# Optimization experiments

Hardware: AMD Instinct MI355X
Metric: run time of the kernel (lower is better)

## Reference

```python
import jax, jax.numpy as jnp
import numpy as np

T = 2048        # q_len (current chunk)
P = 2048        # past KV cache length
HID = 4096      # hidden_size
H = 32          # num_attention_heads
D = HID // H    # head_dim = 128
THETA = 10000.0


def apply_rope(x, pos):
    # x: [H, T, D], pos: [T] int
    half = D // 2
    inv_freq = 1.0 / (THETA ** (jnp.arange(0, half, dtype=jnp.float32) / half))
    ang = pos.astype(jnp.float32)[:, None] * inv_freq[None, :]      # [T, D/2]
    cos = jnp.concatenate([jnp.cos(ang), jnp.cos(ang)], axis=-1)[None]  # [1, T, D]
    sin = jnp.concatenate([jnp.sin(ang), jnp.sin(ang)], axis=-1)[None]
    rot = jnp.concatenate([-x[..., half:], x[..., :half]], axis=-1)
    return x * cos + rot * sin


def setup_inputs() -> dict:
    key = jax.random.key(0)
    ks = jax.random.split(key, 8)
    s = 1.0 / np.sqrt(HID)
    inp = {
        "hidden_states": jax.random.normal(ks[0], (T, HID), dtype=jnp.float32),
        "attention_mask": jnp.triu(jnp.full((T, T), -jnp.inf, dtype=jnp.float32), k=1),
        "Wq": jax.random.normal(ks[1], (HID, HID), dtype=jnp.float32) * s,
        "Wk": jax.random.normal(ks[2], (HID, HID), dtype=jnp.float32) * s,
        "Wv": jax.random.normal(ks[3], (HID, HID), dtype=jnp.float32) * s,
        "Wo": jax.random.normal(ks[4], (HID, HID), dtype=jnp.float32) * s,
        "past_k": jax.random.normal(ks[5], (H, P, D), dtype=jnp.float32),
        "past_v": jax.random.normal(ks[6], (H, P, D), dtype=jnp.float32),
        "position_ids": P + jnp.arange(T, dtype=jnp.int32),
        "past_length": P,
    }
    return inp


def reference(hidden_states, attention_mask, Wq, Wk, Wv, Wo, past_k, past_v,
              position_ids, past_length):
    # QKV projections -> [H, T, D]
    proj = lambda W: (hidden_states @ W).reshape(T, H, D).transpose(1, 0, 2)
    q, k, v = proj(Wq), proj(Wk), proj(Wv)
    q = apply_rope(q, position_ids)
    k = apply_rope(k, position_ids)

    scale = 1.0 / jnp.sqrt(jnp.float32(D))
    # scores against past cache and current chunk (fp32 softmax, as in source)
    past_dots = (jnp.einsum('htd,hsd->hts', q, past_k) * scale).astype(jnp.float32)
    pmask = jnp.where(jnp.arange(P) < past_length, 0.0, -jnp.inf)  # [P]
    past_dots = past_dots + pmask
    cur = ((jnp.einsum('htd,hsd->hts', q, k) * scale) + attention_mask).astype(jnp.float32)

    # online-softmax merge via logsumexp combination
    past_lse = jax.scipy.special.logsumexp(past_dots, axis=-1, keepdims=True)
    cur_lse = jax.scipy.special.logsumexp(cur, axis=-1, keepdims=True)
    tot_lse = jnp.logaddexp(past_lse, cur_lse)
    pw = jnp.exp(past_dots - tot_lse).astype(q.dtype)
    cw = jnp.exp(cur - tot_lse).astype(q.dtype)

    out = jnp.einsum('hts,hsd->htd', pw, past_v) + jnp.einsum('hts,hsd->htd', cw, v)
    out = jnp.where(past_length == 0,
                    jnp.einsum('hts,hsd->htd', jax.nn.softmax(cur, axis=-1).astype(q.dtype), v),
                    out)
    out = out.transpose(1, 0, 2).reshape(T, HID)   # [T, hidden]
    return out @ Wo
```

## Files before the change

### kernel.cpp

```cpp
#include <hip/hip_runtime.h>
#include <cstdint>
#include <cstddef>

#define T_LEN 2048
#define PAST_MAX 2048
#define HID 4096
#define NHEAD 32
#define DHEAD 128

typedef __bf16 bf16_t;
typedef __bf16 bf16x4 __attribute__((ext_vector_type(4)));
typedef __bf16 bf16x8 __attribute__((ext_vector_type(8)));
typedef float  f32x4  __attribute__((ext_vector_type(4)));
typedef float  f32x16 __attribute__((ext_vector_type(16)));
typedef unsigned int u32x4 __attribute__((ext_vector_type(4)));

__device__ __forceinline__ void gload16(const void* g, void* l){
  __builtin_amdgcn_global_load_lds((const __attribute__((address_space(1))) void*)g,
                                   (__attribute__((address_space(3))) void*)l,
                                   16, 0, 0);
}

__device__ __forceinline__ unsigned pack_bf16(float a, float b){
  const unsigned ua = __builtin_bit_cast(unsigned short, (bf16_t)a);
  const unsigned ub = __builtin_bit_cast(unsigned short, (bf16_t)b);
  return ua | (ub << 16);
}

__global__ void cvt2_k(const float* __restrict__ a, bf16_t* __restrict__ ao,
                       const float* __restrict__ b, bf16_t* __restrict__ bo, int n4){
  int i = blockIdx.x * 256 + threadIdx.x;
  if (i < n4){
    const float4 v = ((const float4*)a)[i];
    bf16x4 o = { (bf16_t)v.x, (bf16_t)v.y, (bf16_t)v.z, (bf16_t)v.w };
    ((bf16x4*)ao)[i] = o;
  } else {
    i -= n4;
    const float4 v = ((const float4*)b)[i];
    bf16x4 o = { (bf16_t)v.x, (bf16_t)v.y, (bf16_t)v.z, (bf16_t)v.w };
    ((bf16x4*)bo)[i] = o;
  }
}

__global__ __launch_bounds__(256) void transpose2_k(const float* __restrict__ in,
                                                    bf16_t* __restrict__ out, int R, int C){
  __shared__ float tile[64][65];
  const int r0 = blockIdx.x << 6, c0 = blockIdx.y << 6;
  const size_t bo = (size_t)blockIdx.z * (size_t)R * (size_t)C;
  const int tx = threadIdx.x & 15, ty = threadIdx.x >> 4;
#pragma unroll
  for (int k = 0; k < 4; ++k){
    const float4 v = *(const float4*)(in + bo + (size_t)(r0 + ty + 16*k) * C + c0 + tx*4);
    float* tp = &tile[ty + 16*k][tx*4];
    tp[0] = v.x; tp[1] = v.y; tp[2] = v.z; tp[3] = v.w;
  }
  __syncthreads();
  const int rr0 = (threadIdx.x & 7) * 8;
  const int ccb = threadIdx.x >> 3;
#pragma unroll
  for (int k = 0; k < 2; ++k){
    const int cc = ccb + 32*k;
    bf16x8 o;
#pragma unroll
    for (int j = 0; j < 8; ++j) o[j] = (bf16_t)tile[rr0 + j][cc];
    *(bf16x8*)(out + bo + (size_t)(c0 + cc) * R + r0 + rr0) = o;
  }
}

__global__ __launch_bounds__(256) void transpose3_k(
    const float* __restrict__ s0, const float* __restrict__ s1, const float* __restrict__ s2,
    bf16_t* __restrict__ d0, bf16_t* __restrict__ d1, bf16_t* __restrict__ d2){
  __shared__ float tile[64][65];
  const float* in = (blockIdx.z == 0) ? s0 : (blockIdx.z == 1) ? s1 : s2;
  bf16_t* out = (blockIdx.z == 0) ? d0 : (blockIdx.z == 1) ? d1 : d2;
  const int r0 = blockIdx.x << 6, c0 = blockIdx.y << 6;
  const int tx = threadIdx.x & 15, ty = threadIdx.x >> 4;
#pragma unroll
  for (int k = 0; k < 4; ++k){
    const float4 v = *(const float4*)(in + (size_t)(r0 + ty + 16*k) * HID + c0 + tx*4);
    float* tp = &tile[ty + 16*k][tx*4];
    tp[0] = v.x; tp[1] = v.y; tp[2] = v.z; tp[3] = v.w;
  }
  __syncthreads();
  const int rr0 = (threadIdx.x & 7) * 8;
  const int ccb = threadIdx.x >> 3;
#pragma unroll
  for (int k = 0; k < 2; ++k){
    const int cc = ccb + 32*k;
    bf16x8 o;
#pragma unroll
    for (int j = 0; j < 8; ++j) o[j] = (bf16_t)tile[rr0 + j][cc];
    *(bf16x8*)(out + (size_t)(c0 + cc) * HID + r0 + rr0) = o;
  }
}

__global__ void ropek_k(bf16_t* __restrict__ K, const int* __restrict__ pos){
  const int idx = blockIdx.x * 256 + threadIdx.x;
  const int i = idx & 63;
  const int t = (idx >> 6) & (T_LEN - 1);
  const int h = idx >> 17;
  const size_t base = ((size_t)h * T_LEN + t) * DHEAD;
  const float p = (float)pos[t];
  const float inv = __expf(-(float)i * 0.14391156605212898f);
  const float ang = p * inv;
  float sn, cs;
  sincosf(ang, &sn, &cs);
  const float b0 = (float)K[base + i], b1 = (float)K[base + i + 64];
  K[base + i]      = (bf16_t)(b0 * cs - b1 * sn);
  K[base + i + 64] = (bf16_t)(b1 * cs + b0 * sn);
}

#define QUAD16(AH, NH, BF) \
  __builtin_amdgcn_s_setprio(1); \
  _Pragma("unroll") \
  for (int kk = 0; kk < 2; ++kk){ \
    _Pragma("unroll") \
    for (int mf = 0; mf < 4; ++mf){ \
      _Pragma("unroll") \
      for (int ni = 0; ni < 2; ++ni) \
        acc[(AH)*4 + mf][(NH)*2 + ni] = __builtin_amdgcn_mfma_f32_16x16x32_bf16( \
            af[mf][kk], BF[ni][kk], acc[(AH)*4 + mf][(NH)*2 + ni], 0, 0, 0); \
    } \
  } \
  __builtin_amdgcn_s_setprio(0);

__global__ __launch_bounds__(512, 1) void gemmqkv8_k(
    const bf16_t* __restrict__ A,
    const bf16_t* __restrict__ B0p, const bf16_t* __restrict__ B1p, const bf16_t* __restrict__ B2p,
    bf16_t* __restrict__ OQ, bf16_t* __restrict__ OK2, bf16_t* __restrict__ OVT, int cpx)
{
  const int bid = blockIdx.x;
  const int wg  = (bid & 7) * cpx + (bid >> 3);
  const int mt  = wg & 7;
  const int nt  = wg >> 3;
  const int z   = nt >> 4;
  const int m0  = mt << 8;
  const int n0  = (nt & 15) << 8;
  const bf16_t* __restrict__ B = (z == 0) ? B0p : (z == 1) ? B1p : B2p;

  const int tid = threadIdx.x;
  const int wv = tid >> 6, lane = tid & 63, lm = lane & 15, g = lane >> 4;
  const int wr = wv >> 2, wc = wv & 3;

  __shared__ __align__(16) char smem[131072];

  const f32x4 fzero = {0.f, 0.f, 0.f, 0.f};
  f32x4 acc[8][4];
#pragma unroll
  for (int i = 0; i < 8; ++i)
#pragma unroll
    for (int j = 0; j < 4; ++j) acc[i][j] = fzero;

  int arow_[2], brow_[2], jcol_[2];
#pragma unroll
  for (int i = 0; i < 2; ++i){
    const int c  = i * 512 + tid;
    const int rl = c >> 3;
    const int j  = (c & 7) ^ (rl & 7);
    arow_[i] = m0 + ((rl >> 6) << 7) + (rl & 63);
    brow_[i] = n0 + ((rl >> 5) << 6) + (rl & 31);
    jcol_[i] = j << 3;
  }
  const int ldst0 = ((0 * 512 + wv * 64) << 4);
  const int ldst1 = ((1 * 512 + wv * 64) << 4);

  auto stgA = [&](int kt, int ah){
    if ((unsigned)kt < 64u){
      char* dst = smem + (kt & 1) * 65536 + ah * 16384;
      const bf16_t* base = A + (size_t)kt * 64;
      gload16(base + (size_t)(arow_[0] + ah * 64) * HID + jcol_[0], dst + ldst0);
      gload16(base + (size_t)(arow_[1] + ah * 64) * HID + jcol_[1], dst + ldst1);
    }
  };
  auto stgB = [&](int kt, int nh){
    if ((unsigned)kt < 64u){
      char* dst = smem + (kt & 1) * 65536 + 32768 + nh * 16384;
      const bf16_t* base = B + (size_t)kt * 64;
      gload16(base + (size_t)(brow_[0] + nh * 32) * HID + jcol_[0], dst + ldst0);
      gload16(base + (size_t)(brow_[1] + nh * 32) * HID + jcol_[1], dst + ldst1);
    }
  };

  const int koff0 = ((0 + g) ^ (lm & 7)) << 4;
  const int koff1 = ((4 + g) ^ (lm & 7)) << 4;
  const int abase = ((wr << 6) + lm) << 7;
  const int bbase = ((wc << 5) + lm) << 7;

  stgA(0, 0); stgB(0, 0); stgB(0, 1); stgA(0, 1);
  stgA(1, 0); stgB(1, 0); stgB(1, 1);
  asm volatile("s_waitcnt vmcnt(6)" ::: "memory");
  __builtin_amdgcn_s_barrier();

  bf16x8 af[4][2], b0f[2][2], b1f[2][2];

  for (int kt = 0; kt < 64; ++kt){
    char* buf = smem + (kt & 1) * 65536;

#pragma unroll
    for (int mf = 0; mf < 4; ++mf){
      af[mf][0] = *(const bf16x8*)(buf + abase + mf * 2048 + koff0);
      af[mf][1] = *(const bf16x8*)(buf + abase + mf * 2048 + koff1);
    }
#pragma unroll
    for (int ni = 0; ni < 2; ++ni){
      b0f[ni][0] = *(const bf16x8*)(buf + 32768 + bbase + ni * 2048 + koff0);
      b0f[ni][1] = *(const bf16x8*)(buf + 32768 + bbase + ni * 2048 + koff1);
    }
    stgA(kt + 1, 1);
    __builtin_amdgcn_sched_barrier(0);
    __builtin_amdgcn_s_barrier();
    asm volatile("s_waitcnt lgkmcnt(0)" ::: "memory");
    __builtin_amdgcn_sched_barrier(0);
    QUAD16(0, 0, b0f)
    __builtin_amdgcn_s_barrier();

#pragma unroll
    for (int ni = 0; ni < 2; ++ni){
      b1f[ni][0] = *(const bf16x8*)(buf + 49152 + bbase + ni * 2048 + koff0);
      b1f[ni][1] = *(const bf16x8*)(buf + 49152 + bbase + ni * 2048 + koff1);
    }
    stgA(kt + 2, 0);
    __builtin_amdgcn_sched_barrier(0);
    __builtin_amdgcn_s_barrier();
    asm volatile("s_waitcnt lgkmcnt(0)" ::: "memory");
    __builtin_amdgcn_sched_barrier(0);
    QUAD16(0, 1, b1f)
    __builtin_amdgcn_s_barrier();

#pragma unroll
    for (int mf = 0; mf < 4; ++mf){
      af[mf][0] = *(const bf16x8*)(buf + 16384 + abase + mf * 2048 + koff0);
      af[mf][1] = *(const bf16x8*)(buf + 16384 + abase + mf * 2048 + koff1);
    }
    stgB(kt + 2, 0);
    __builtin_amdgcn_sched_barrier(0);
    __builtin_amdgcn_s_barrier();
    asm volatile("s_waitcnt lgkmcnt(0)" ::: "memory");
    __builtin_amdgcn_sched_barrier(0);
    QUAD16(1, 1, b1f)
    __builtin_amdgcn_s_barrier();

    stgB(kt + 2, 1);
    if (kt < 60) asm volatile("s_waitcnt vmcnt(6)" ::: "memory");
    else         asm volatile("s_waitcnt vmcnt(0)" ::: "memory");
    __builtin_amdgcn_sched_barrier(0);
    __builtin_amdgcn_s_barrier();
    QUAD16(1, 0, b0f)
    __builtin_amdgcn_s_barrier();
  }

#pragma unroll
  for (int ni4 = 0; ni4 < 4; ++ni4){
    const int col = n0 + wc * 64 + (ni4 >> 1) * 32 + (ni4 & 1) * 16 + lm;
    const int hh = col >> 7, dd = col & 127;
#pragma unroll
    for (int mf8 = 0; mf8 < 8; ++mf8){
      const int trow0 = m0 + wr * 128 + (mf8 >> 2) * 64 + (mf8 & 3) * 16 + g * 4;
      if (z == 2){
        bf16x4 v4 = { (bf16_t)acc[mf8][ni4][0], (bf16_t)acc[mf8][ni4][1],
                      (bf16_t)acc[mf8][ni4][2], (bf16_t)acc[mf8][ni4][3] };
        *(bf16x4*)(OVT + ((size_t)hh * DHEAD + dd) * T_LEN + trow0) = v4;
      } else {
        bf16_t* ob = (z == 1) ? OK2 : OQ;
#pragma unroll
        for (int r = 0; r < 4; ++r)
          ob[((size_t)hh * T_LEN + trow0 + r) * DHEAD + dd] = (bf16_t)acc[mf8][ni4][r];
      }
    }
  }
}

__global__ __launch_bounds__(512, 1) void gemm4p_k(
    const bf16_t* __restrict__ A, const bf16_t* __restrict__ B,
    float* __restrict__ OF, int cpx)
{
  const int bid = blockIdx.x;
  const int wg  = (bid & 7) * cpx + (bid >> 3);
  const int mt  = wg & 7;
  const int nt  = wg >> 3;
  const int m0  = mt << 8;
  const int n0  = nt << 7;

  const int tid = threadIdx.x;
  const int wv = tid >> 6, lane = tid & 63, lm = lane & 15, g = lane >> 4;
  const int wr = wv >> 1, wc = wv & 1;

  __shared__ __align__(16) char smem[98304];

  const f32x4 fzero = {0.f, 0.f, 0.f, 0.f};
  f32x4 acc[4][4];
#pragma unroll
  for (int i = 0; i < 4; ++i)
#pragma unroll
    for (int j = 0; j < 4; ++j) acc[i][j] = fzero;

  int srow[2], schk[2];
#pragma unroll
  for (int i = 0; i < 2; ++i){
    const int c = i * 512 + tid;
    srow[i] = c >> 3;
    schk[i] = (c & 7) ^ (srow[i] & 7);
  }
  const int sdst0 = ((0 * 512 + wv * 64) << 4);
  const int sdst1 = ((1 * 512 + wv * 64) << 4);

  auto stg = [&](int kt, int op){
    if (kt < 64){
      char* dst = smem + (kt & 1) * 49152 + op * 16384;
      const bf16_t* base = (op < 2) ? A + (size_t)(m0 + (op << 7)) * HID
                                    : B + (size_t)n0 * HID;
      base += kt * 64;
      gload16(base + (size_t)srow[0] * HID + schk[0] * 8, dst + sdst0);
      gload16(base + (size_t)srow[1] * HID + schk[1] * 8, dst + sdst1);
    }
  };

  const int koff0 = ((g)     ^ (lm & 7)) << 4;
  const int koff1 = ((4 + g) ^ (lm & 7)) << 4;
  const int abase = ((wr >> 1) << 14) + ((((wr & 1) << 6) + lm) << 7);
  const int bbase = 32768 + ((((wc << 6)) + lm) << 7);

  bf16x8 bfr[4][2];
  auto dsB = [&](int buf){
    const char* p = smem + buf * 49152 + bbase;
#pragma unroll
    for (int ni = 0; ni < 4; ++ni){
      bfr[ni][0] = *(const bf16x8*)(p + ni * 2048 + koff0);
      bfr[ni][1] = *(const bf16x8*)(p + ni * 2048 + koff1);
    }
  };

  stg(0, 2);
  stg(0, 0); stg(0, 1);
  stg(1, 2);
  asm volatile("s_waitcnt vmcnt(2)" ::: "memory");
  __builtin_amdgcn_s_barrier();

  for (int t = 0; t < 32; ++t){
    const int c0 = 2 * t, c1 = 2 * t + 1;
    const bool last = (t == 31);

#pragma unroll
    for (int half = 0; half < 2; ++half){
      const char* bufp = smem + half * 49152;
      bf16x8 afr[2][2];
      dsB(half);
#pragma unroll
      for (int mf = 0; mf < 2; ++mf){
        afr[mf][0] = *(const bf16x8*)(bufp + abase + mf * 2048 + koff0);
        afr[mf][1] = *(const bf16x8*)(bufp + abase + mf * 2048 + koff1);
      }
      if (half == 0){ stg(c1, 0); stg(c1, 1); }
      else          { stg(c0 + 2, 0); stg(c0 + 2, 1); }
      __builtin_amdgcn_s_barrier();
      asm volatile("s_waitcnt lgkmcnt(0)" ::: "memory");
      __builtin_amdgcn_s_setprio(1);
#pragma unroll
      for (int kk = 0; kk < 2; ++kk)
#pragma unroll
        for (int mf = 0; mf < 2; ++mf)
#pragma unroll
          for (int ni = 0; ni < 4; ++ni)
            acc[mf][ni] = __builtin_amdgcn_mfma_f32_16x16x32_bf16(afr[mf][kk], bfr[ni][kk], acc[mf][ni], 0, 0, 0);
      __builtin_amdgcn_s_setprio(0);
      __builtin_amdgcn_s_barrier();

#pragma unroll
      for (int mf = 0; mf < 2; ++mf){
        afr[mf][0] = *(const bf16x8*)(bufp + abase + (mf + 2) * 2048 + koff0);
        afr[mf][1] = *(const bf16x8*)(bufp + abase + (mf + 2) * 2048 + koff1);
      }
      if (half == 0) stg(c0 + 2, 2);
      else           stg(c1 + 2, 2);
      if (last) asm volatile("s_waitcnt vmcnt(0)" ::: "memory");
      else      asm volatile("s_waitcnt vmcnt(2)" ::: "memory");
      __builtin_amdgcn_s_barrier();
      asm volatile("s_waitcnt lgkmcnt(0)" ::: "memory");
      __builtin_amdgcn_s_setprio(1);
#pragma unroll
      for (int kk = 0; kk < 2; ++kk)
#pragma unroll
        for (int mf = 0; mf < 2; ++mf)
#pragma unroll
          for (int ni = 0; ni < 4; ++ni)
            acc[mf + 2][ni] = __builtin_amdgcn_mfma_f32_16x16x32_bf16(afr[mf][kk], bfr[ni][kk], acc[mf + 2][ni], 0, 0, 0);
      __builtin_amdgcn_s_setprio(0);
      __builtin_amdgcn_s_barrier();
    }
  }

#pragma unroll
  for (int ni = 0; ni < 4; ++ni){
    const int col = n0 + wc * 64 + ni * 16 + lm;
#pragma unroll
    for (int mf = 0; mf < 4; ++mf)
#pragma unroll
      for (int r = 0; r < 4; ++r){
        const int trow = m0 + wr * 64 + mf * 16 + g * 4 + r;
        OF[(size_t)trow * HID + col] = acc[mf][ni][r];
      }
  }
}

__global__ __launch_bounds__(256, 2) void attn2_k(
    const bf16_t* __restrict__ Q,
    const bf16_t* __restrict__ Kc,
    const bf16_t* __restrict__ VTc,
    const bf16_t* __restrict__ Kp,
    const bf16_t* __restrict__ VTp,
    bf16_t* __restrict__ Ctx,
    const int* __restrict__ plen_p,
    const int* __restrict__ pos)
{
  const int bid = blockIdx.x;
  const int xcd = bid & 7;
  const int k   = bid >> 3;
  const int ho  = k >> 4;
  const int qraw= k & 15;
  const int h   = (xcd << 2) | ho;
  const int qb  = (ho & 2) ? (15 - qraw) : qraw;

  const int tid = threadIdx.x;
  const int w = tid >> 6, lane = tid & 63, l31 = lane & 31, hi = lane >> 5;
  const int qw0 = qb * 128 + w * 32;
  const int qrow = qw0 + l31;
  const int plen = plen_p[0];
  const int npast = (plen + 63) >> 6;
  const int NT = npast + 2 * qb + 2;

  __shared__ __align__(16) char smem[65536 + 512];
  float* lred = (float*)(smem + 65536);

  const bf16_t* qbase = Q + ((size_t)h * T_LEN + qrow) * DHEAD;
  bf16x8 qf[8];
#pragma unroll
  for (int dc = 0; dc < 8; ++dc)
    qf[dc] = *(const bf16x8*)(qbase + dc * 16 + 8 * hi);
  {
    const float ppos = (float)pos[qrow];
    const float qs = 0.08838834764831845f;
#pragma unroll
    for (int dc = 0; dc < 4; ++dc)
#pragma unroll
      for (int j = 0; j < 8; ++j){
        const int fi = dc * 16 + 8 * hi + j;
        const float invf = __expf(-(float)fi * 0.14391156605212898f);
        float sn, cs;
        sincosf(ppos * invf, &sn, &cs);
        const float a0 = (float)qf[dc][j], a1 = (float)qf[dc + 4][j];
        qf[dc][j]     = (bf16_t)((a0 * cs - a1 * sn) * qs);
        qf[dc + 4][j] = (bf16_t)((a1 * cs + a0 * sn) * qs);
      }
  }
  __builtin_amdgcn_sched_barrier(0);

  const f32x16 fz = {0.f,0.f,0.f,0.f,0.f,0.f,0.f,0.f,0.f,0.f,0.f,0.f,0.f,0.f,0.f,0.f};
  f32x16 o[4] = {fz, fz, fz, fz};
  float m = -1e30f, l = 0.f;

  auto stage = [&](int t, int buf){
    const bf16_t* kb; const bf16_t* vb;
    if (t < npast){
      const int s0 = t * 64;
      kb = Kp  + ((size_t)h * PAST_MAX + s0) * DHEAD;
      vb = VTp + (size_t)h * DHEAD * PAST_MAX + s0;
    } else {
      const int s0 = (t - npast) * 64;
      kb = Kc  + ((size_t)h * T_LEN + s0) * DHEAD;
      vb = VTc + (size_t)h * DHEAD * T_LEN + s0;
    }
    char* kl = smem + buf * 32768;
    char* vl = kl + 16384;
#pragma unroll
    for (int i = 0; i < 4; ++i){
      const int c = i * 256 + w * 64 + lane;
      const int krow = c >> 4, kcol = c & 15;
      gload16(kb + (size_t)krow * DHEAD + ((kcol ^ (krow & 7)) << 3), kl + (i * 256 + w * 64) * 16);
      const int vrow = c >> 3, vcol = c & 7;
      gload16(vb + (size_t)vrow * 2048 + ((vcol ^ (vrow & 7)) << 3), vl + (i * 256 + w * 64) * 16);
    }
  };

  stage(0, 0);
  __builtin_amdgcn_sched_barrier(0);

  for (int t = 0; t < NT; ++t){
    const int cur = t & 1;
    if (t + 1 < NT){
      stage(t + 1, cur ^ 1);
      asm volatile("s_waitcnt vmcnt(8)" ::: "memory");
    } else {
      asm volatile("s_waitcnt vmcnt(0)" ::: "memory");
    }
    __builtin_amdgcn_sched_barrier(0);
    __builtin_amdgcn_s_barrier();
    __builtin_amdgcn_sched_barrier(0);

    const bool isc = (t >= npast);
    const int s0c = (t - npast) * 64;
    const bool active = !isc || (s0c <= qw0 + 31);

    if (active){
      char* kl = smem + cur * 32768;
      char* vl = kl + 16384;

      f32x16 sacc[2] = {fz, fz};
      __builtin_amdgcn_s_setprio(1);
#pragma unroll
      for (int kvh = 0; kvh < 2; ++kvh){
        const int krow = (kvh << 5) + l31;
        const int kbo = krow << 8;
        const int sw = (krow & 7) << 4;
#pragma unroll
        for (int dc = 0; dc < 8; ++dc){
          const bf16x8 kf = *(const bf16x8*)(kl + kbo + ((dc * 32 + 16 * hi) ^ sw));
          sacc[kvh] = __builtin_amdgcn_mfma_f32_32x32x16_bf16(kf, qf[dc], sacc[kvh], 0, 0, 0);
        }
      }
      __builtin_amdgcn_s_setprio(0);

      const bool mcur  = isc && (s0c + 63 > qw0);
      const bool mpast = !isc && ((t + 1) * 64 > plen);
      float pv[2][16];
      float pm = -1e30f;
      if (mcur | mpast){
#pragma unroll
        for (int kvh = 0; kvh < 2; ++kvh)
#pragma unroll
          for (int r = 0; r < 16; ++r){
            float x = sacc[kvh][r];
            const int kvoff = (kvh << 5) + (r & 3) + 8 * (r >> 2) + 4 * hi;
            if (mcur  && (s0c + kvoff >  qrow)) x = -1e30f;
            if (mpast && (t * 64 + kvoff >= plen)) x = -1e30f;
            pv[kvh][r] = x;
            pm = fmaxf(pm, x);
          }
      } else {
#pragma unroll
        for (int kvh = 0; kvh < 2; ++kvh)
#pragma unroll
          for (int r = 0; r < 16; ++r){
            pv[kvh][r] = sacc[kvh][r];
            pm = fmaxf(pm, sacc[kvh][r]);
          }
      }
      pm = fmaxf(pm, __shfl_xor(pm, 32));

      if (!__all(pm - m <= 8.f)){
        const float mn = fmaxf(m, pm);
        const float corr = __expf(m - mn);
        m = mn;
        l *= corr;
        if (hi == 0) lred[(w << 5) + l31] = corr;
        asm volatile("s_waitcnt lgkmcnt(0)" ::: "memory");
#pragma unroll
        for (int r = 0; r < 16; ++r){
          const float cc = lred[(w << 5) + (r & 3) + 8 * (r >> 2) + 4 * hi];
#pragma unroll
          for (int nb = 0; nb < 4; ++nb) o[nb][r] *= cc;
        }
      }

      float sum = 0.f;
#pragma unroll
      for (int kvh = 0; kvh < 2; ++kvh)
#pragma unroll
        for (int r = 0; r < 16; ++r){
          const float pe = __expf(pv[kvh][r] - m);
          pv[kvh][r] = pe;
          sum += pe;
        }
      sum += __shfl_xor(sum, 32);
      l += sum;

      unsigned wds[2][8];
#pragma unroll
      for (int kvh = 0; kvh < 2; ++kvh)
#pragma unroll
        for (int i = 0; i < 8; ++i)
          wds[kvh][i] = pack_bf16(pv[kvh][2 * i], pv[kvh][2 * i + 1]);

      bf16x8 pf[4];
#pragma unroll
      for (int ks = 0; ks < 4; ++ks){
        const int s = ks & 1, kvh = ks >> 1;
        const unsigned a0 = hi ? wds[kvh][4 * s]     : wds[kvh][4 * s + 2];
        const unsigned a1 = hi ? wds[kvh][4 * s + 1] : wds[kvh][4 * s + 3];
        const unsigned z0 = (unsigned)__shfl_xor((int)a0, 32);
        const unsigned z1 = (unsigned)__shfl_xor((int)a1, 32);
        u32x4 fw;
        fw[0] = hi ? z0 : wds[kvh][4 * s];
        fw[1] = hi ? z1 : wds[kvh][4 * s + 1];
        fw[2] = hi ? wds[kvh][4 * s + 2] : z0;
        fw[3] = hi ? wds[kvh][4 * s + 3] : z1;
        pf[ks] = __builtin_bit_cast(bf16x8, fw);
      }

      __builtin_amdgcn_s_setprio(1);
#pragma unroll
      for (int ks = 0; ks < 4; ++ks)
#pragma unroll
        for (int nb = 0; nb < 4; ++nb){
          const int vrow = (nb << 5) + l31;
          const bf16x8 vf = *(const bf16x8*)(vl + (vrow << 7) + ((ks * 32 + 16 * hi) ^ ((vrow & 7) << 4)));
          o[nb] = __builtin_amdgcn_mfma_f32_32x32x16_bf16(pf[ks], vf, o[nb], 0, 0, 0);
        }
      __builtin_amdgcn_s_setprio(0);
    }
    __builtin_amdgcn_sched_barrier(0);
    __builtin_amdgcn_s_barrier();
  }

  if (hi == 0) lred[(w << 5) + l31] = l;
  asm volatile("s_waitcnt lgkmcnt(0)" ::: "memory");
#pragma unroll
  for (int r = 0; r < 16; ++r){
    const int cr = (r & 3) + 8 * (r >> 2) + 4 * hi;
    const float li = 1.f / lred[(w << 5) + cr];
    const int trow = qw0 + cr;
    bf16_t* cb = Ctx + (size_t)trow * HID + h * DHEAD + l31;
#pragma unroll
    for (int nb = 0; nb < 4; ++nb)
      cb[nb << 5] = (bf16_t)(o[nb][r] * li);
  }
}

extern "C" void kernel_launch(void* const* d_in, const int* in_sizes, int n_in,
                              void* d_out, int out_size, void* d_ws, size_t ws_size,
                              hipStream_t stream)
{
  const float* X   = (const float*)d_in[0];
  const float* Wq  = (const float*)d_in[2];
  const float* Wk  = (const float*)d_in[3];
  const float* Wv  = (const float*)d_in[4];
  const float* Wo  = (const float*)d_in[5];
  const float* PKi = (const float*)d_in[6];
  const float* PVi = (const float*)d_in[7];
  const int* POS   = (const int*)d_in[8];
  const int* PLEN  = (const int*)d_in[9];
  float* OUT = (float*)d_out;

  char* ws = (char*)d_ws;
  const size_t SZ_XB  = (size_t)T_LEN * HID * 2;
  const size_t SZ_W   = (size_t)HID * HID * 2;
  const size_t SZ_HTD = (size_t)NHEAD * T_LEN * DHEAD * 2;

  bf16_t* XB  = (bf16_t*)(ws);
  bf16_t* WT0 = (bf16_t*)(ws + SZ_XB);
  bf16_t* WT1 = (bf16_t*)(ws + SZ_XB + SZ_W);
  bf16_t* WT2 = (bf16_t*)(ws + SZ_XB + 2 * SZ_W);
  char* p = ws + SZ_XB + 3 * SZ_W;
  bf16_t* QB   = (bf16_t*)p; p += SZ_HTD;
  bf16_t* KB   = (bf16_t*)p; p += SZ_HTD;
  bf16_t* VTB  = (bf16_t*)p; p += SZ_HTD;
  bf16_t* KPB  = (bf16_t*)p; p += SZ_HTD;
  bf16_t* VPTB = (bf16_t*)p; p += SZ_HTD;
  bf16_t* CTX  = (bf16_t*)p; p += SZ_HTD;
  bf16_t* WOT  = QB;

  dim3 blk256(256);
  dim3 blk512(512);
  cvt2_k<<<16384, blk256, 0, stream>>>(X, XB, PKi, KPB, T_LEN * HID / 4);
  transpose3_k<<<dim3(64,64,3), blk256, 0, stream>>>(Wq, Wk, Wv, WT0, WT1, WT2);
  transpose2_k<<<dim3(32,2,32), blk256, 0, stream>>>(PVi, VPTB, PAST_MAX, DHEAD);

  gemmqkv8_k<<<384, blk512, 0, stream>>>(XB, WT0, WT1, WT2, QB, KB, VTB, 48);
  ropek_k<<<16384, blk256, 0, stream>>>(KB, POS);
  attn2_k<<<512, blk256, 0, stream>>>(QB, KB, VTB, KPB, VPTB, CTX, PLEN, POS);

  transpose2_k<<<dim3(64,64,1), blk256, 0, stream>>>(Wo, WOT, HID, HID);
  gemm4p_k<<<256, blk512, 0, stream>>>(CTX, WOT, OUT, 32);
}
```

Measured before the change: 562.8 us.

## Retile fused QKV GEMM to 128x384 tiles over concatenated weights

The QKV projection GEMM moves from 256x256 tiles (384 blocks) to 128x384 tiles (512 blocks), treating the three transposed weight matrices as one contiguous N=12288 operand. Each k-step loads one A slice and three B slices, and the output column decides whether results go to Q, K, or transposed V. The goal is better load balance across the CUs, since 512 blocks divide more evenly than 384, at the cost of lower arithmetic intensity per tile. It relies on WT0, WT1 and WT2 sitting contiguously in the workspace.

Result: faster. 535.4 us (-4.9%).

```diff
diff --git a/kernel.cpp b/kernel.cpp
--- a/kernel.cpp
+++ b/kernel.cpp
@@ -110,7 +110,7 @@
   K[base + i + 64] = (bf16_t)(b1 * cs + b0 * sn);
 }
 
-#define QUAD16(AH, NH, BF) \
+#define QUAD384(PR, BF) \
   __builtin_amdgcn_s_setprio(1); \
   _Pragma("unroll") \
   for (int kk = 0; kk < 2; ++kk){ \
@@ -118,25 +118,23 @@
     for (int mf = 0; mf < 4; ++mf){ \
       _Pragma("unroll") \
       for (int ni = 0; ni < 2; ++ni) \
-        acc[(AH)*4 + mf][(NH)*2 + ni] = __builtin_amdgcn_mfma_f32_16x16x32_bf16( \
-            af[mf][kk], BF[ni][kk], acc[(AH)*4 + mf][(NH)*2 + ni], 0, 0, 0); \
+        acc[mf][(PR)*2 + ni] = __builtin_amdgcn_mfma_f32_16x16x32_bf16( \
+            af[mf][kk], BF[ni][kk], acc[mf][(PR)*2 + ni], 0, 0, 0); \
     } \
   } \
   __builtin_amdgcn_s_setprio(0);
 
-__global__ __launch_bounds__(512, 1) void gemmqkv8_k(
+__global__ __launch_bounds__(512, 1) void gemmqkv384_k(
     const bf16_t* __restrict__ A,
-    const bf16_t* __restrict__ B0p, const bf16_t* __restrict__ B1p, const bf16_t* __restrict__ B2p,
-    bf16_t* __restrict__ OQ, bf16_t* __restrict__ OK2, bf16_t* __restrict__ OVT, int cpx)
+    const bf16_t* __restrict__ Bc,
+    bf16_t* __restrict__ OQ, bf16_t* __restrict__ OK2, bf16_t* __restrict__ OVT)
 {
   const int bid = blockIdx.x;
-  const int wg  = (bid & 7) * cpx + (bid >> 3);
-  const int mt  = wg & 7;
-  const int nt  = wg >> 3;
-  const int z   = nt >> 4;
-  const int m0  = mt << 8;
-  const int n0  = (nt & 15) << 8;
-  const bf16_t* __restrict__ B = (z == 0) ? B0p : (z == 1) ? B1p : B2p;
+  const int wg  = (bid & 7) * 64 + (bid >> 3);
+  const int mt  = wg & 15;
+  const int nt  = wg >> 4;
+  const int m0  = mt << 7;
+  const int n0g = nt * 384;
 
   const int tid = threadIdx.x;
   const int wv = tid >> 6, lane = tid & 63, lm = lane & 15, g = lane >> 4;
@@ -145,40 +143,35 @@
   __shared__ __align__(16) char smem[131072];
 
   const f32x4 fzero = {0.f, 0.f, 0.f, 0.f};
-  f32x4 acc[8][4];
-#pragma unroll
-  for (int i = 0; i < 8; ++i)
-#pragma unroll
-    for (int j = 0; j < 4; ++j) acc[i][j] = fzero;
-
-  int arow_[2], brow_[2], jcol_[2];
+  f32x4 acc[4][6];
+#pragma unroll
+  for (int i = 0; i < 4; ++i)
+#pragma unroll
+    for (int j = 0; j < 6; ++j) acc[i][j] = fzero;
+
+  size_t aoff[2], boff[2];
 #pragma unroll
   for (int i = 0; i < 2; ++i){
-    const int c  = i * 512 + tid;
-    const int rl = c >> 3;
-    const int j  = (c & 7) ^ (rl & 7);
-    arow_[i] = m0 + ((rl >> 6) << 7) + (rl & 63);
-    brow_[i] = n0 + ((rl >> 5) << 6) + (rl & 31);
-    jcol_[i] = j << 3;
-  }
-  const int ldst0 = ((0 * 512 + wv * 64) << 4);
-  const int ldst1 = ((1 * 512 + wv * 64) << 4);
-
-  auto stgA = [&](int kt, int ah){
-    if ((unsigned)kt < 64u){
-      char* dst = smem + (kt & 1) * 65536 + ah * 16384;
-      const bf16_t* base = A + (size_t)kt * 64;
-      gload16(base + (size_t)(arow_[0] + ah * 64) * HID + jcol_[0], dst + ldst0);
-      gload16(base + (size_t)(arow_[1] + ah * 64) * HID + jcol_[1], dst + ldst1);
-    }
+    const int c = i * 512 + tid;
+    const int u = c >> 3;
+    const int j = ((c & 7) ^ (u & 7)) << 3;
+    aoff[i] = (size_t)(m0 + u) * HID + j;
+    const int bcol = (u >> 5) * 96 + (u & 31);
+    boff[i] = (size_t)(n0g + bcol) * HID + j;
+  }
+  const int ldst0 = (wv * 64) << 4;
+  const int ldst1 = (512 + wv * 64) << 4;
+
+  auto stgA = [&](char* buf, int kt){
+    const bf16_t* src = A + (size_t)kt * 64;
+    gload16(src + aoff[0], buf + ldst0);
+    gload16(src + aoff[1], buf + ldst1);
   };
-  auto stgB = [&](int kt, int nh){
-    if ((unsigned)kt < 64u){
-      char* dst = smem + (kt & 1) * 65536 + 32768 + nh * 16384;
-      const bf16_t* base = B + (size_t)kt * 64;
-      gload16(base + (size_t)(brow_[0] + nh * 32) * HID + jcol_[0], dst + ldst0);
-      gload16(base + (size_t)(brow_[1] + nh * 32) * HID + jcol_[1], dst + ldst1);
-    }
+  auto stgB = [&](char* buf, int kt, int pr){
+    const bf16_t* src = Bc + (size_t)kt * 64 + (size_t)pr * (32 * HID);
+    char* dst = buf + 16384 + pr * 16384;
+    gload16(src + boff[0], dst + ldst0);
+    gload16(src + boff[1], dst + ldst1);
   };
 
   const int koff0 = ((0 + g) ^ (lm & 7)) << 4;
@@ -186,15 +179,16 @@
   const int abase = ((wr << 6) + lm) << 7;
   const int bbase = ((wc << 5) + lm) << 7;
 
-  stgA(0, 0); stgB(0, 0); stgB(0, 1); stgA(0, 1);
-  stgA(1, 0); stgB(1, 0); stgB(1, 1);
+  stgA(smem, 0); stgB(smem, 0, 0); stgB(smem, 0, 1); stgB(smem, 0, 2);
+  stgA(smem + 65536, 1); stgB(smem + 65536, 1, 0); stgB(smem + 65536, 1, 1);
   asm volatile("s_waitcnt vmcnt(6)" ::: "memory");
   __builtin_amdgcn_s_barrier();
 
-  bf16x8 af[4][2], b0f[2][2], b1f[2][2];
+  bf16x8 af[4][2], bf[2][2];
 
   for (int kt = 0; kt < 64; ++kt){
-    char* buf = smem + (kt & 1) * 65536;
+    char* buf  = smem + (kt & 1) * 65536;
+    char* obuf = smem + ((kt + 1) & 1) * 65536;
 
 #pragma unroll
     for (int mf = 0; mf < 4; ++mf){
@@ -203,71 +197,71 @@
     }
 #pragma unroll
     for (int ni = 0; ni < 2; ++ni){
-      b0f[ni][0] = *(const bf16x8*)(buf + 32768 + bbase + ni * 2048 + koff0);
-      b0f[ni][1] = *(const bf16x8*)(buf + 32768 + bbase + ni * 2048 + koff1);
-    }
-    stgA(kt + 1, 1);
+      bf[ni][0] = *(const bf16x8*)(buf + 16384 + bbase + ni * 2048 + koff0);
+      bf[ni][1] = *(const bf16x8*)(buf + 16384 + bbase + ni * 2048 + koff1);
+    }
+    if (kt + 1 < 64) stgB(obuf, kt + 1, 2);
     __builtin_amdgcn_sched_barrier(0);
     __builtin_amdgcn_s_barrier();
     asm volatile("s_waitcnt lgkmcnt(0)" ::: "memory");
     __builtin_amdgcn_sched_barrier(0);
-    QUAD16(0, 0, b0f)
+    QUAD384(0, bf)
     __builtin_amdgcn_s_barrier();
 
 #pragma unroll
     for (int ni = 0; ni < 2; ++ni){
-      b1f[ni][0] = *(const bf16x8*)(buf + 49152 + bbase + ni * 2048 + koff0);
-      b1f[ni][1] = *(const bf16x8*)(buf + 49152 + bbase + ni * 2048 + koff1);
-    }
-    stgA(kt + 2, 0);
+      bf[ni][0] = *(const bf16x8*)(buf + 32768 + bbase + ni * 2048 + koff0);
+      bf[ni][1] = *(const bf16x8*)(buf + 32768 + bbase + ni * 2048 + koff1);
+    }
+    if (kt + 2 < 64) stgA(buf, kt + 2);
     __builtin_amdgcn_sched_barrier(0);
     __builtin_amdgcn_s_barrier();
     asm volatile("s_waitcnt lgkmcnt(0)" ::: "memory");
     __builtin_amdgcn_sched_barrier(0);
-    QUAD16(0, 1, b1f)
-    __builtin_amdgcn_s_barrier();
-
-#pragma unroll
-    for (int mf = 0; mf < 4; ++mf){
-      af[mf][0] = *(const bf16x8*)(buf + 16384 + abase + mf * 2048 + koff0);
-      af[mf][1] = *(const bf16x8*)(buf + 16384 + abase + mf * 2048 + koff1);
-    }
-    stgB(kt + 2, 0);
+    QUAD384(1, bf)
+    __builtin_amdgcn_s_barrier();
+
+#pragma unroll
+    for (int ni = 0; ni < 2; ++ni){
+      bf[ni][0] = *(const bf16x8*)(buf + 49152 + bbase + ni * 2048 + koff0);
+      bf[ni][1] = *(const bf16x8*)(buf + 49152 + bbase + ni * 2048 + koff1);
+    }
+    if (kt + 2 < 64){ stgB(buf, kt + 2, 0); stgB(buf, kt + 2, 1); }
     __builtin_amdgcn_sched_barrier(0);
     __builtin_amdgcn_s_barrier();
     asm volatile("s_waitcnt lgkmcnt(0)" ::: "memory");
     __builtin_amdgcn_sched_barrier(0);
-    QUAD16(1, 1, b1f)
-    __builtin_amdgcn_s_barrier();
-
-    stgB(kt + 2, 1);
-    if (kt < 60) asm volatile("s_waitcnt vmcnt(6)" ::: "memory");
-    else         asm volatile("s_waitcnt vmcnt(0)" ::: "memory");
-    __builtin_amdgcn_sched_barrier(0);
-    __builtin_amdgcn_s_barrier();
-    QUAD16(1, 0, b0f)
-    __builtin_amdgcn_s_barrier();
-  }
-
-#pragma unroll
-  for (int ni4 = 0; ni4 < 4; ++ni4){
-    const int col = n0 + wc * 64 + (ni4 >> 1) * 32 + (ni4 & 1) * 16 + lm;
-    const int hh = col >> 7, dd = col & 127;
-#pragma unroll
-    for (int mf8 = 0; mf8 < 8; ++mf8){
-      const int trow0 = m0 + wr * 128 + (mf8 >> 2) * 64 + (mf8 & 3) * 16 + g * 4;
-      if (z == 2){
-        bf16x4 v4 = { (bf16_t)acc[mf8][ni4][0], (bf16_t)acc[mf8][ni4][1],
-                      (bf16_t)acc[mf8][ni4][2], (bf16_t)acc[mf8][ni4][3] };
-        *(bf16x4*)(OVT + ((size_t)hh * DHEAD + dd) * T_LEN + trow0) = v4;
-      } else {
-        bf16_t* ob = (z == 1) ? OK2 : OQ;
-#pragma unroll
-        for (int r = 0; r < 4; ++r)
-          ob[((size_t)hh * T_LEN + trow0 + r) * DHEAD + dd] = (bf16_t)acc[mf8][ni4][r];
-      }
-    }
-  }
+    QUAD384(2, bf)
+    if (kt <= 61) asm volatile("s_waitcnt vmcnt(6)" ::: "memory");
+    else          asm volatile("s_waitcnt vmcnt(0)" ::: "memory");
+    __builtin_amdgcn_sched_barrier(0);
+    __builtin_amdgcn_s_barrier();
+  }
+
+#pragma unroll
+  for (int pr = 0; pr < 3; ++pr)
+#pragma unroll
+    for (int ni = 0; ni < 2; ++ni){
+      const int colg = n0g + wc * 96 + pr * 32 + ni * 16 + lm;
+      const int z  = colg >> 12;
+      const int wi = colg & 4095;
+      const int hh = wi >> 7, dd = wi & 127;
+      const int ai = pr * 2 + ni;
+#pragma unroll
+      for (int mf = 0; mf < 4; ++mf){
+        const int trow0 = m0 + wr * 64 + mf * 16 + g * 4;
+        if (z == 2){
+          bf16x4 v4 = { (bf16_t)acc[mf][ai][0], (bf16_t)acc[mf][ai][1],
+                        (bf16_t)acc[mf][ai][2], (bf16_t)acc[mf][ai][3] };
+          *(bf16x4*)(OVT + ((size_t)hh * DHEAD + dd) * T_LEN + trow0) = v4;
+        } else {
+          bf16_t* ob = z ? OK2 : OQ;
+#pragma unroll
+          for (int r = 0; r < 4; ++r)
+            ob[((size_t)hh * T_LEN + trow0 + r) * DHEAD + dd] = (bf16_t)acc[mf][ai][r];
+        }
+      }
+    }
 }
 
 __global__ __launch_bounds__(512, 1) void gemm4p_k(
@@ -664,7 +658,7 @@
   transpose3_k<<<dim3(64,64,3), blk256, 0, stream>>>(Wq, Wk, Wv, WT0, WT1, WT2);
   transpose2_k<<<dim3(32,2,32), blk256, 0, stream>>>(PVi, VPTB, PAST_MAX, DHEAD);
 
-  gemmqkv8_k<<<384, blk512, 0, stream>>>(XB, WT0, WT1, WT2, QB, KB, VTB, 48);
+  gemmqkv384_k<<<512, blk512, 0, stream>>>(XB, WT0, QB, KB, VTB);
   ropek_k<<<16384, blk256, 0, stream>>>(KB, POS);
   attn2_k<<<512, blk256, 0, stream>>>(QB, KB, VTB, KPB, VPTB, CTX, PLEN, POS);
 
```
